# Performance work log

Measured on AMD Instinct MI355X. Metric: run time of the kernel, lower is better.

Reference implementation:

```python
import jax, jax.numpy as jnp
import numpy as np

IM_SIZE = 128  # imSize: image is [B,1,IM_SIZE,IM_SIZE]


def setup_inputs() -> dict:
    key = jax.random.key(0)
    # channel 0: image to reconstruct; channel 1: passthrough 'others' channel
    inp = jax.random.normal(key, (16, 2, IM_SIZE, IM_SIZE), dtype=jnp.float32)
    return {"input": inp}


def reference(input):
    S = IM_SIZE
    x = input[:, 0]        # [B,H,W] real image (input[:, :1] in torch)
    others = input[:, 1:]  # extra channels, concatenated back at the end

    # RFFT: torch.rfft(x, 2, onesided=False, normalized=False) == fft2
    K = jnp.fft.fft2(x)    # [B,H,W] complex64

    # seperate_mask keeps only k-space column i for output channel i:
    # masked[b,i,h,w] = K[b,h,w] * (w == i)
    eye = jnp.eye(S, dtype=jnp.float32)
    masked = K[:, None, :, :] * eye[None, :, None, :]  # [B,S,H,W]

    # IFFT: torch.ifft(..., normalized=False) == standard 1/N-normalized ifft2;
    # module keeps channel 0 of the (real, imag) pair -> real part.
    imgs = jnp.fft.ifft2(masked).real.astype(input.dtype)  # [B,S,H,W]

    return jnp.concatenate([imgs, others], axis=1)  # [B, S + C-1, H, W]
```

## Files before the change

kernel.cpp:

```cpp
#include <hip/hip_runtime.h>
#include <math.h>

#define S 128
constexpr float TWO_PI_OVER_S = 6.283185307179586f / 128.0f;

__global__ void dft_rows(const float* __restrict__ in, float2* __restrict__ F) {
    const int by = blockIdx.x;
    const int b  = by >> 7;
    const int y  = by & (S - 1);
    const int s  = threadIdx.x;

    __shared__ float row[S];
    row[s] = in[((b * 2 + 0) * S + y) * S + s];
    __syncthreads();

    float re = 0.f, im = 0.f;
#pragma unroll 4
    for (int v = 0; v < S; ++v) {
        const int k = (s * v) & (S - 1);
        float sn, c;
        __sincosf((float)k * TWO_PI_OVER_S, &sn, &c);
        const float xv = row[v];
        re = fmaf(xv, c, re);
        im = fmaf(xv, -sn, im);
    }
    F[by * S + s] = make_float2(re, im);
}

__global__ void modulate(const float2* __restrict__ F, float* __restrict__ out) {
    const int gid = blockIdx.x * blockDim.x + threadIdx.x;
    const int x0  = (gid & 31) * 4;
    int rem = gid >> 5;
    const int y = rem & (S - 1); rem >>= 7;
    const int s = rem & (S - 1);
    const int b = rem >> 7;

    const float2 f  = F[(b * S + y) * S + s];
    const float  re = f.x * (1.0f / S);
    const float  im = f.y * (1.0f / S);

    float4 o;
    float* op = &o.x;
#pragma unroll
    for (int j = 0; j < 4; ++j) {
        const int k = (s * (x0 + j)) & (S - 1);
        float sn, c;
        __sincosf((float)k * TWO_PI_OVER_S, &sn, &c);
        op[j] = re * c - im * sn;
    }
    *reinterpret_cast<float4*>(&out[((b * 129 + s) * S + y) * S + x0]) = o;
}

__global__ void copy_others(const float* __restrict__ in, float* __restrict__ out) {
    const int gid = blockIdx.x * blockDim.x + threadIdx.x;
    const int xq  = (gid & 31) * 4;
    int rem = gid >> 5;
    const int y = rem & (S - 1);
    const int b = rem >> 7;
    const float4 v = *reinterpret_cast<const float4*>(&in[((b * 2 + 1) * S + y) * S + xq]);
    *reinterpret_cast<float4*>(&out[((b * 129 + 128) * S + y) * S + xq]) = v;
}

extern "C" void kernel_launch(void* const* d_in, const int* in_sizes, int n_in,
                              void* d_out, int out_size, void* d_ws, size_t ws_size,
                              hipStream_t stream) {
    const float* in  = (const float*)d_in[0];
    float*       out = (float*)d_out;
    float2*      F   = (float2*)d_ws;

    const int B = 16;

    dft_rows<<<B * S, S, 0, stream>>>(in, F);

    const int total_threads = B * S * S * (S / 4);
    modulate<<<total_threads / 256, 256, 0, stream>>>(F, out);

    copy_others<<<(B * S * (S / 4)) / 256, 256, 0, stream>>>(in, out);
}
```

Measured before the change: 144.6 us.

## Use shared twiddle tables, transpose DFT output, and fuse passthrough copy into modulate

The row DFT now reads cos/sin from shared-memory tables instead of calling sincos per term, and stores its output transposed so each modulate block can load one contiguous column of frequency values. Modulate becomes one block per (batch, column) that caches the column and the twiddles in shared memory and writes a full 128x128 output plane. The passthrough copy is folded into extra blocks of the same launch, removing one kernel launch. Total output size is unchanged, so the write-bound main kernel is expected to shift only modestly; the transposed store in dft_rows is strided.

```diff
diff --git a/kernel.cpp b/kernel.cpp
--- a/kernel.cpp
+++ b/kernel.cpp
@@ -2,63 +2,89 @@
 #include <math.h>
 
 #define S 128
-constexpr float TWO_PI_OVER_S = 6.283185307179586f / 128.0f;
+#define NB 16
+constexpr float STEP = 6.283185307179586f / 128.0f;
 
-__global__ void dft_rows(const float* __restrict__ in, float2* __restrict__ F) {
+__global__ void dft_rows(const float* __restrict__ in, float2* __restrict__ Ft) {
     const int by = blockIdx.x;
     const int b  = by >> 7;
     const int y  = by & (S - 1);
     const int s  = threadIdx.x;
 
     __shared__ float row[S];
+    __shared__ float cosT[S], sinT[S];
     row[s] = in[((b * 2 + 0) * S + y) * S + s];
+    float sn, cs;
+    __sincosf((float)s * STEP, &sn, &cs);
+    cosT[s] = cs;
+    sinT[s] = sn;
     __syncthreads();
 
     float re = 0.f, im = 0.f;
-#pragma unroll 4
+#pragma unroll 8
     for (int v = 0; v < S; ++v) {
         const int k = (s * v) & (S - 1);
-        float sn, c;
-        __sincosf((float)k * TWO_PI_OVER_S, &sn, &c);
         const float xv = row[v];
-        re = fmaf(xv, c, re);
-        im = fmaf(xv, -sn, im);
+        re = fmaf(xv,  cosT[k], re);
+        im = fmaf(xv, -sinT[k], im);
     }
-    F[by * S + s] = make_float2(re, im);
+    Ft[(b * S + s) * S + y] = make_float2(re, im);
 }
 
-__global__ void modulate(const float2* __restrict__ F, float* __restrict__ out) {
-    const int gid = blockIdx.x * blockDim.x + threadIdx.x;
-    const int x0  = (gid & 31) * 4;
-    int rem = gid >> 5;
-    const int y = rem & (S - 1); rem >>= 7;
-    const int s = rem & (S - 1);
-    const int b = rem >> 7;
+__global__ void modulate(const float2* __restrict__ Ft, const float* __restrict__ in,
+                         float* __restrict__ out) {
+    const int blk = blockIdx.x;
+    const int t   = threadIdx.x;
 
-    const float2 f  = F[(b * S + y) * S + s];
-    const float  re = f.x * (1.0f / S);
-    const float  im = f.y * (1.0f / S);
+    if (blk >= NB * S) {
+        const int b = blk - NB * S;
+        const float4* src = (const float4*)&in[((b * 2 + 1) * S) * S];
+        float4*       dst = (float4*)&out[((b * 129 + S) * S) * S];
+#pragma unroll
+        for (int i = 0; i < 16; ++i)
+            dst[i * 256 + t] = src[i * 256 + t];
+        return;
+    }
 
-    float4 o;
-    float* op = &o.x;
+    const int b = blk >> 7;
+    const int s = blk & (S - 1);
+
+    __shared__ float2 Fs[S];
+    __shared__ float  cosT[S], sinT[S];
+    if (t < S) {
+        Fs[t] = Ft[(b * S + s) * S + t];
+        float sn, cs;
+        __sincosf((float)t * STEP, &sn, &cs);
+        cosT[t] = cs;
+        sinT[t] = sn;
+    }
+    __syncthreads();
+
+    const int x0 = (t & 31) * 4;
+    const int y0 = t >> 5;
+
+    float mc[4], ms[4];
 #pragma unroll
     for (int j = 0; j < 4; ++j) {
         const int k = (s * (x0 + j)) & (S - 1);
-        float sn, c;
-        __sincosf((float)k * TWO_PI_OVER_S, &sn, &c);
-        op[j] = re * c - im * sn;
+        mc[j] = cosT[k];
+        ms[j] = sinT[k];
     }
-    *reinterpret_cast<float4*>(&out[((b * 129 + s) * S + y) * S + x0]) = o;
-}
 
-__global__ void copy_others(const float* __restrict__ in, float* __restrict__ out) {
-    const int gid = blockIdx.x * blockDim.x + threadIdx.x;
-    const int xq  = (gid & 31) * 4;
-    int rem = gid >> 5;
-    const int y = rem & (S - 1);
-    const int b = rem >> 7;
-    const float4 v = *reinterpret_cast<const float4*>(&in[((b * 2 + 1) * S + y) * S + xq]);
-    *reinterpret_cast<float4*>(&out[((b * 129 + 128) * S + y) * S + xq]) = v;
+    float* obase = &out[((b * 129 + s) * S) * S];
+#pragma unroll
+    for (int i = 0; i < 16; ++i) {
+        const int y = y0 + i * 8;
+        const float2 f  = Fs[y];
+        const float  re = f.x * (1.0f / S);
+        const float  im = f.y * (1.0f / S);
+        float4 o;
+        o.x = re * mc[0] - im * ms[0];
+        o.y = re * mc[1] - im * ms[1];
+        o.z = re * mc[2] - im * ms[2];
+        o.w = re * mc[3] - im * ms[3];
+        *(float4*)&obase[y * S + x0] = o;
+    }
 }
 
 extern "C" void kernel_launch(void* const* d_in, const int* in_sizes, int n_in,
@@ -66,14 +92,8 @@
                               hipStream_t stream) {
     const float* in  = (const float*)d_in[0];
     float*       out = (float*)d_out;
-    float2*      F   = (float2*)d_ws;
+    float2*      Ft  = (float2*)d_ws;
 
-    const int B = 16;
-
-    dft_rows<<<B * S, S, 0, stream>>>(in, F);
-
-    const int total_threads = B * S * S * (S / 4);
-    modulate<<<total_threads / 256, 256, 0, stream>>>(F, out);
-
-    copy_others<<<(B * S * (S / 4)) / 256, 256, 0, stream>>>(in, out);
+    dft_rows<<<NB * S, S, 0, stream>>>(in, Ft);
+    modulate<<<NB * S + NB, 256, 0, stream>>>(Ft, in, out);
 }
```

After: 150.5 us. 4.1% more time.
